# Optimization experiments

Hardware: AMD Instinct MI355X
Metric: run time of the kernel (lower is better)

## Reference

```python
import jax, jax.numpy as jnp
import numpy as np

N_NODES = 10000
N_EDGES = 320000
IN_FEATS = 500
CONV_DIMS = [500, 256, 256]
FC_DIMS = [256, 128, 40]
BN_EPS = 1e-5


def setup_inputs() -> dict:
    key = jax.random.key(0)
    ks = jax.random.split(key, 16)
    inp = {
        "x": jax.random.normal(ks[0], (N_NODES, IN_FEATS), dtype=jnp.float32),
        "edge_index": jax.random.randint(ks[1], (2, N_EDGES), 0, N_NODES, dtype=jnp.int64),
    }
    # conv layer params: Linear W [in,out], b [out]; BatchNorm gamma/beta [out]
    ki = 2
    for li in range(len(CONV_DIMS) - 1):
        d_in, d_out = CONV_DIMS[li], CONV_DIMS[li + 1]
        s = 1.0 / np.sqrt(d_in)
        inp[f"conv_W{li}"] = jax.random.uniform(ks[ki], (d_in, d_out), jnp.float32, -s, s); ki += 1
        inp[f"conv_b{li}"] = jax.random.uniform(ks[ki], (d_out,), jnp.float32, -s, s); ki += 1
        inp[f"bn_g{li}"] = jnp.ones((d_out,), jnp.float32)
        inp[f"bn_b{li}"] = jnp.zeros((d_out,), jnp.float32)
    for li in range(len(FC_DIMS) - 1):
        d_in, d_out = FC_DIMS[li], FC_DIMS[li + 1]
        s = 1.0 / np.sqrt(d_in)
        inp[f"fc_W{li}"] = jax.random.uniform(ks[ki], (d_in, d_out), jnp.float32, -s, s); ki += 1
        inp[f"fc_b{li}"] = jax.random.uniform(ks[ki], (d_out,), jnp.float32, -s, s); ki += 1
    return inp


def _degree(edge_index, n, dtype):
    # Faithful to: A = eye(N); A[i,j] = 1 per edge (set semantics dedupes repeats).
    A = jnp.eye(n, dtype=dtype).at[edge_index[0], edge_index[1]].set(1.0)
    return A.sum(axis=1)  # deg_i = rowsum of A


def _batchnorm(h, g, b):
    # training-mode BatchNorm1d: batch stats, biased variance
    mean = h.mean(axis=0)
    var = h.var(axis=0)
    return (h - mean) * jax.lax.rsqrt(var + BN_EPS) * g + b


def reference(x, edge_index, conv_W0, conv_b0, bn_g0, bn_b0,
              conv_W1, conv_b1, bn_g1, bn_b1,
              fc_W0, fc_b0, fc_W1, fc_b1):
    n = x.shape[0]
    deg = _degree(edge_index, n, x.dtype)
    # D = sqrt(diag(deg)) is a diagonal matrix, so elementwise D*A*D = diag(deg);
    # mm(D*A*D, x) == deg[:, None] * x (exactly the original math).
    h = x
    for W, b, g, beta in ((conv_W0, conv_b0, bn_g0, bn_b0),
                          (conv_W1, conv_b1, bn_g1, bn_b1)):
        h = (deg[:, None] * h) @ W + b
        h = jax.nn.relu(h)
        h = _batchnorm(h, g, beta)
        # dropout: identity at inference
    for W, b in ((fc_W0, fc_b0), (fc_W1, fc_b1)):
        h = jax.nn.relu(h @ W + b)  # original appends ReLU after every fc, incl. last
    return h
```

## Files before the change

### kernel.cpp

```cpp
#include <hip/hip_runtime.h>

#define NN 10000
#define NE 320000
#define ROW_WORDS 320
#define MP 10112
#define BN_EPS 1e-5f

typedef __attribute__((ext_vector_type(8))) short short8;
typedef __attribute__((ext_vector_type(4))) float f32x4;
typedef unsigned short u16;

__device__ __forceinline__ void split1(float v, u16& h, u16& l) {
    unsigned int u = __float_as_uint(v);
    h = (u16)(u >> 16);
    float hf = __uint_as_float(u & 0xFFFF0000u);
    l = (u16)(__float_as_uint(v - hf) >> 16);
}

__device__ __forceinline__ void gll16(const void* g, void* l) {
    __builtin_amdgcn_global_load_lds(
        (const __attribute__((address_space(1))) unsigned int*)g,
        (__attribute__((address_space(3))) unsigned int*)l, 16, 0, 0);
}

__global__ void scatter_bits(const int* __restrict__ ei, unsigned int* __restrict__ bitmap) {
    int t = blockIdx.x * blockDim.x + threadIdx.x;
    if (t < NE) {
        int i = ei[t];
        int j = ei[NE + t];
        atomicOr(&bitmap[i * ROW_WORDS + (j >> 5)], 1u << (j & 31));
    } else if (t < NE + NN) {
        int i = t - NE;
        atomicOr(&bitmap[i * ROW_WORDS + (i >> 5)], 1u << (i & 31));
    }
}

__device__ void splitW_dev(const float* __restrict__ W, int K, int N, int Kp, int Np,
                           u16* __restrict__ Wt, int bx, int by, char* smem) {
    float (*tile)[65] = (float(*)[65])smem;
    int t = threadIdx.x;
    int bk = bx * 64, bn = by * 64;
    #pragma unroll
    for (int p = 0; p < 4; ++p) {
        int kk = (t >> 4) + p * 16;
        int nc = (t & 15) * 4;
        int k = bk + kk;
        float4 v = {0.f, 0.f, 0.f, 0.f};
        if (k < K && bn + nc + 3 < N)
            v = *(const float4*)&W[(size_t)k * N + bn + nc];
        tile[kk][nc] = v.x; tile[kk][nc + 1] = v.y;
        tile[kk][nc + 2] = v.z; tile[kk][nc + 3] = v.w;
    }
    __syncthreads();
    int nn = t >> 2;
    int kk0 = (t & 3) * 16;
    u16 hs[16], ls[16];
    #pragma unroll
    for (int j = 0; j < 16; ++j) split1(tile[kk0 + j][nn], hs[j], ls[j]);
    size_t ob = (size_t)(bn + nn) * Kp + bk + kk0;
    size_t lo = (size_t)Np * Kp;
    *(short8*)&Wt[ob] = *(short8*)hs;
    *(short8*)&Wt[ob + 8] = *(short8*)&hs[8];
    *(short8*)&Wt[lo + ob] = *(short8*)ls;
    *(short8*)&Wt[lo + ob + 8] = *(short8*)&ls[8];
}

__device__ void xsplit_dev(const float* __restrict__ x, u16* __restrict__ xs, int gblk) {
    int t = threadIdx.x;
    int r0 = gblk * 16 + (t >> 4);
    int l = t & 15;
    u16* xlo = xs + (size_t)MP * 512;
    #pragma unroll
    for (int j = 0; j < 8; ++j) {
        int k = (l + j * 16) * 4;
        float vals[4] = {0.f, 0.f, 0.f, 0.f};
        if (r0 < NN && k < 500) {
            float4 v = *(const float4*)&x[(size_t)r0 * 500 + k];
            vals[0] = v.x; vals[1] = v.y; vals[2] = v.z; vals[3] = v.w;
        }
        ushort4 hs, ls;
        split1(vals[0], hs.x, ls.x); split1(vals[1], hs.y, ls.y);
        split1(vals[2], hs.z, ls.z); split1(vals[3], hs.w, ls.w);
        *(ushort4*)&xs[(size_t)r0 * 512 + k] = hs;
        *(ushort4*)&xlo[(size_t)r0 * 512 + k] = ls;
    }
}

__device__ void degree_dev(const unsigned int* __restrict__ bitmap, float* __restrict__ deg,
                           int gblk) {
    int t = threadIdx.x;
    int r = gblk * 16 + (t >> 4), l = t & 15;
    int cnt = 0;
    if (r < NN)
        for (int wd = l; wd < ROW_WORDS; wd += 16)
            cnt += __popc(bitmap[(size_t)r * ROW_WORDS + wd]);
    cnt += __shfl_down(cnt, 8, 16);
    cnt += __shfl_down(cnt, 4, 16);
    cnt += __shfl_down(cnt, 2, 16);
    cnt += __shfl_down(cnt, 1, 16);
    if (l == 0 && r < NN) deg[r] = (float)cnt;
}

__global__ __launch_bounds__(256)
void prep(const unsigned int* __restrict__ bitmap, const float* __restrict__ x,
          const float* __restrict__ W0, const float* __restrict__ fW1,
          float* __restrict__ deg, u16* __restrict__ xs,
          u16* __restrict__ W0t, u16* __restrict__ fW1t) {
    __shared__ char smem[16704];
    int b = blockIdx.x;
    if (b < 632) {
        degree_dev(bitmap, deg, b);
        xsplit_dev(x, xs, b);
    } else if (b < 664) {
        int idx = b - 632;
        splitW_dev(W0, 500, 256, 512, 256, W0t, idx & 7, idx >> 3, smem);
    } else {
        splitW_dev(fW1, 128, 40, 128, 64, fW1t, b - 664, 0, smem);
    }
}

__global__ __launch_bounds__(256, 3)
void conv0_gemm(const u16* __restrict__ Ahi, const u16* __restrict__ Alo,
                const u16* __restrict__ Bhi, const u16* __restrict__ Blo,
                const float* __restrict__ bias, const float* __restrict__ deg,
                float* __restrict__ stats, u16* __restrict__ Ohi, u16* __restrict__ Olo) {
    __shared__ char smem[32768];
    const int Kp = 512, M = NN, No = 256;
    const int t = threadIdx.x;
    const int lane = t & 63;
    const int w = t >> 6;
    const int q = lane >> 4;
    const int l16 = lane & 15;
    const int m7 = l16 & 7;
    const int row0 = blockIdx.y * 64;
    const int col0 = blockIdx.x * 64;

    const u16* bases[4] = {Ahi, Alo, Bhi, Blo};
    const u16* srcs[8];
    unsigned dstoff[8];
    #pragma unroll
    for (int i = 0; i < 8; ++i) {
        int gi = w + i * 4;
        int reg = i >> 1;
        int j = gi & 7;
        int rb = (reg < 2) ? row0 : col0;
        int r = j * 8 + (lane >> 3);
        int c = (lane & 7) ^ (r & 7);
        srcs[i] = bases[reg] + (size_t)(rb + r) * Kp + c * 8;
        dstoff[i] = reg * 8192 + j * 1024;
    }

    f32x4 acc[4];
    #pragma unroll
    for (int s = 0; s < 4; ++s) acc[s] = (f32x4){0.f, 0.f, 0.f, 0.f};

    #pragma unroll
    for (int i = 0; i < 8; ++i) { gll16(srcs[i], smem + dstoff[i]); srcs[i] += 64; }

    for (int k0 = 0; k0 < Kp; k0 += 64) {
        __syncthreads();
        short8 ah[2], al[2], bh[2][4], bl[2][4];
        #pragma unroll
        for (int kc = 0; kc < 2; ++kc) {
            int aoff = (w * 16 + l16) * 128 + (((kc * 4 + q) ^ m7) * 16);
            ah[kc] = *(const short8*)(smem + aoff);
            al[kc] = *(const short8*)(smem + 8192 + aoff);
            #pragma unroll
            for (int s = 0; s < 4; ++s) {
                int boff = (s * 16 + l16) * 128 + (((kc * 4 + q) ^ m7) * 16);
                bh[kc][s] = *(const short8*)(smem + 16384 + boff);
                bl[kc][s] = *(const short8*)(smem + 24576 + boff);
            }
        }
        __syncthreads();
        if (k0 + 64 < Kp) {
            #pragma unroll
            for (int i = 0; i < 8; ++i) { gll16(srcs[i], smem + dstoff[i]); srcs[i] += 64; }
        }
        #pragma unroll
        for (int kc = 0; kc < 2; ++kc)
            #pragma unroll
            for (int s = 0; s < 4; ++s) {
                acc[s] = __builtin_amdgcn_mfma_f32_16x16x32_bf16(al[kc], bh[kc][s], acc[s], 0, 0, 0);
                acc[s] = __builtin_amdgcn_mfma_f32_16x16x32_bf16(ah[kc], bl[kc][s], acc[s], 0, 0, 0);
                acc[s] = __builtin_amdgcn_mfma_f32_16x16x32_bf16(ah[kc], bh[kc][s], acc[s], 0, 0, 0);
            }
    }

    int growb = row0 + w * 16 + q * 4;
    float dgv[4];
    #pragma unroll
    for (int r = 0; r < 4; ++r) dgv[r] = (growb + r < M) ? deg[growb + r] : 0.f;
    #pragma unroll
    for (int s = 0; s < 4; ++s) {
        int gc = col0 + s * 16 + l16;
        float bia = bias[gc];
        float s_sum = 0.f, ss_sum = 0.f;
        #pragma unroll
        for (int r = 0; r < 4; ++r) {
            int grow = growb + r;
            bool real = grow < M;
            float v = fmaxf(fmaf(dgv[r], acc[s][r], bia), 0.f);
            if (!real) v = 0.f;
            s_sum += v; ss_sum += v * v;
            float vo = v * dgv[r];
            u16 h, l; split1(vo, h, l);
            Ohi[(size_t)grow * No + gc] = h;
            Olo[(size_t)grow * No + gc] = l;
        }
        s_sum  += __shfl_xor(s_sum, 16);  s_sum  += __shfl_xor(s_sum, 32);
        ss_sum += __shfl_xor(ss_sum, 16); ss_sum += __shfl_xor(ss_sum, 32);
        if (lane < 16) {
            atomicAdd(&stats[gc], s_sum);
            atomicAdd(&stats[256 + gc], ss_sum);
        }
    }
}

__global__ __launch_bounds__(256, 2)
void conv1_fold(const u16* __restrict__ Ahi, const u16* __restrict__ Alo,
                const float* __restrict__ W1, const float* __restrict__ stats0,
                const float* __restrict__ g0, const float* __restrict__ bb0,
                const float* __restrict__ b1, const float* __restrict__ deg,
                float* __restrict__ stats1, u16* __restrict__ Ohi, u16* __restrict__ Olo) {
    __shared__ char smem[32768];
    __shared__ float scl[256], sh[256], cred[256], cvec[64];
    const int Kp = 256, M = NN, No = 256;
    const int t = threadIdx.x;
    const int lane = t & 63;
    const int w = t >> 6;
    const int q = lane >> 4;
    const int l16 = lane & 15;
    const int m7 = l16 & 7;
    const int row0 = blockIdx.y * 64;
    const int col0 = blockIdx.x * 64;

    const u16* srcs[4];
    unsigned dstoff[4];
    #pragma unroll
    for (int i = 0; i < 4; ++i) {
        int gi = w + i * 4;
        int plane = gi >> 3, j = gi & 7;
        int r = j * 8 + (lane >> 3);
        int c = (lane & 7) ^ (r & 7);
        srcs[i] = (plane ? Alo : Ahi) + (size_t)(row0 + r) * Kp + c * 8;
        dstoff[i] = plane * 8192 + j * 1024;
    }
    #pragma unroll
    for (int i = 0; i < 4; ++i) { gll16(srcs[i], smem + dstoff[i]); srcs[i] += 64; }

    {
        float mean = stats0[t] * (1.f / NN);
        float var = stats0[256 + t] * (1.f / NN) - mean * mean;
        float s = g0[t] * rsqrtf(var + BN_EPS);
        scl[t] = s;
        sh[t] = bb0[t] - mean * s;
    }
    __syncthreads();
    {
        float s = 0.f;
        int n = col0 + (t & 63);
        #pragma unroll 8
        for (int k = (t >> 6); k < 256; k += 4)
            s += sh[k] * W1[(size_t)k * 256 + n];
        cred[t] = s;
        __syncthreads();
        if (t < 64) cvec[t] = cred[t] + cred[t + 64] + cred[t + 128] + cred[t + 192];
    }
    const int bn = t & 63;
    const int kb = (t >> 6) * 16;
    const int ch0 = (t >> 6) * 2;
    float vals[16];
    {
        const float* wp = W1 + (size_t)kb * 256 + col0 + bn;
        #pragma unroll
        for (int i = 0; i < 16; ++i) vals[i] = wp[(size_t)i * 256] * scl[kb + i];
    }

    f32x4 acc[4];
    #pragma unroll
    for (int s = 0; s < 4; ++s) acc[s] = (f32x4){0.f, 0.f, 0.f, 0.f};

    for (int k0 = 0; k0 < Kp; k0 += 64) {
        {
            u16 hs[16], ls[16];
            #pragma unroll
            for (int i = 0; i < 16; ++i) split1(vals[i], hs[i], ls[i]);
            unsigned o0 = bn * 128 + ((ch0 ^ (bn & 7)) * 16);
            unsigned o1 = bn * 128 + (((ch0 + 1) ^ (bn & 7)) * 16);
            *(short8*)(smem + 16384 + o0) = *(short8*)&hs[0];
            *(short8*)(smem + 16384 + o1) = *(short8*)&hs[8];
            *(short8*)(smem + 24576 + o0) = *(short8*)&ls[0];
            *(short8*)(smem + 24576 + o1) = *(short8*)&ls[8];
        }
        __syncthreads();
        short8 ah[2], al[2], bh[2][4], bl[2][4];
        #pragma unroll
        for (int kc = 0; kc < 2; ++kc) {
            int aoff = (w * 16 + l16) * 128 + (((kc * 4 + q) ^ m7) * 16);
            ah[kc] = *(const short8*)(smem + aoff);
            al[kc] = *(const short8*)(smem + 8192 + aoff);
            #pragma unroll
            for (int s = 0; s < 4; ++s) {
                int boff = (s * 16 + l16) * 128 + (((kc * 4 + q) ^ m7) * 16);
                bh[kc][s] = *(const short8*)(smem + 16384 + boff);
                bl[kc][s] = *(const short8*)(smem + 24576 + boff);
            }
        }
        __syncthreads();
        if (k0 + 64 < Kp) {
            #pragma unroll
            for (int i = 0; i < 4; ++i) { gll16(srcs[i], smem + dstoff[i]); srcs[i] += 64; }
            const float* wp = W1 + (size_t)(k0 + 64 + kb) * 256 + col0 + bn;
            #pragma unroll
            for (int i = 0; i < 16; ++i) vals[i] = wp[(size_t)i * 256] * scl[k0 + 64 + kb + i];
        }
        #pragma unroll
        for (int kc = 0; kc < 2; ++kc)
            #pragma unroll
            for (int s = 0; s < 4; ++s) {
                acc[s] = __builtin_amdgcn_mfma_f32_16x16x32_bf16(al[kc], bh[kc][s], acc[s], 0, 0, 0);
                acc[s] = __builtin_amdgcn_mfma_f32_16x16x32_bf16(ah[kc], bl[kc][s], acc[s], 0, 0, 0);
                acc[s] = __builtin_amdgcn_mfma_f32_16x16x32_bf16(ah[kc], bh[kc][s], acc[s], 0, 0, 0);
            }
    }

    int growb = row0 + w * 16 + q * 4;
    float dgv[4];
    #pragma unroll
    for (int r = 0; r < 4; ++r) dgv[r] = (growb + r < M) ? deg[growb + r] : 0.f;
    #pragma unroll
    for (int s = 0; s < 4; ++s) {
        int gc = col0 + s * 16 + l16;
        float bia = b1[gc];
        float cv = cvec[s * 16 + l16];
        float s_sum = 0.f, ss_sum = 0.f;
        #pragma unroll
        for (int r = 0; r < 4; ++r) {
            int grow = growb + r;
            bool real = grow < M;
            float v = fmaxf(fmaf(dgv[r], cv, acc[s][r] + bia), 0.f);
            if (!real) v = 0.f;
            s_sum += v; ss_sum += v * v;
            u16 h, l; split1(v, h, l);
            Ohi[(size_t)grow * No + gc] = h;
            Olo[(size_t)grow * No + gc] = l;
        }
        s_sum  += __shfl_xor(s_sum, 16);  s_sum  += __shfl_xor(s_sum, 32);
        ss_sum += __shfl_xor(ss_sum, 16); ss_sum += __shfl_xor(ss_sum, 32);
        if (lane < 16) {
            atomicAdd(&stats1[gc], s_sum);
            atomicAdd(&stats1[256 + gc], ss_sum);
        }
    }
}

__global__ __launch_bounds__(256, 2)
void fc0_fold(const u16* __restrict__ Ahi, const u16* __restrict__ Alo,
              const float* __restrict__ fW0, const float* __restrict__ stats1,
              const float* __restrict__ g1, const float* __restrict__ bb1,
              const float* __restrict__ fb0,
              u16* __restrict__ Ohi, u16* __restrict__ Olo) {
    __shared__ char smem[32768];
    __shared__ float scl[256], sh[256], cred[256], biasf[64];
    const int Kp = 256, M = NN, No = 128;
    const int t = threadIdx.x;
    const int lane = t & 63;
    const int w = t >> 6;
    const int q = lane >> 4;
    const int l16 = lane & 15;
    const int m7 = l16 & 7;
    const int row0 = blockIdx.y * 64;
    const int col0 = blockIdx.x * 64;

    const u16* srcs[4];
    unsigned dstoff[4];
    #pragma unroll
    for (int i = 0; i < 4; ++i) {
        int gi = w + i * 4;
        int plane = gi >> 3, j = gi & 7;
        int r = j * 8 + (lane >> 3);
        int c = (lane & 7) ^ (r & 7);
        srcs[i] = (plane ? Alo : Ahi) + (size_t)(row0 + r) * Kp + c * 8;
        dstoff[i] = plane * 8192 + j * 1024;
    }
    #pragma unroll
    for (int i = 0; i < 4; ++i) { gll16(srcs[i], smem + dstoff[i]); srcs[i] += 64; }

    {
        float mean = stats1[t] * (1.f / NN);
        float var = stats1[256 + t] * (1.f / NN) - mean * mean;
        float s = g1[t] * rsqrtf(var + BN_EPS);
        scl[t] = s;
        sh[t] = bb1[t] - mean * s;
    }
    __syncthreads();
    {
        float s = 0.f;
        int n = col0 + (t & 63);
        #pragma unroll 8
        for (int k = (t >> 6); k < 256; k += 4)
            s += sh[k] * fW0[(size_t)k * 128 + n];
        cred[t] = s;
        __syncthreads();
        if (t < 64)
            biasf[t] = fb0[col0 + t] + cred[t] + cred[t + 64] + cred[t + 128] + cred[t + 192];
    }
    const int bn = t & 63;
    const int kb = (t >> 6) * 16;
    const int ch0 = (t >> 6) * 2;
    float vals[16];
    {
        const float* wp = fW0 + (size_t)kb * 128 + col0 + bn;
        #pragma unroll
        for (int i = 0; i < 16; ++i) vals[i] = wp[(size_t)i * 128] * scl[kb + i];
    }

    f32x4 acc[4];
    #pragma unroll
    for (int s = 0; s < 4; ++s) acc[s] = (f32x4){0.f, 0.f, 0.f, 0.f};

    for (int k0 = 0; k0 < Kp; k0 += 64) {
        {
            u16 hs[16], ls[16];
            #pragma unroll
            for (int i = 0; i < 16; ++i) split1(vals[i], hs[i], ls[i]);
            unsigned o0 = bn * 128 + ((ch0 ^ (bn & 7)) * 16);
            unsigned o1 = bn * 128 + (((ch0 + 1) ^ (bn & 7)) * 16);
            *(short8*)(smem + 16384 + o0) = *(short8*)&hs[0];
            *(short8*)(smem + 16384 + o1) = *(short8*)&hs[8];
            *(short8*)(smem + 24576 + o0) = *(short8*)&ls[0];
            *(short8*)(smem + 24576 + o1) = *(short8*)&ls[8];
        }
        __syncthreads();
        short8 ah[2], al[2], bh[2][4], bl[2][4];
        #pragma unroll
        for (int kc = 0; kc < 2; ++kc) {
            int aoff = (w * 16 + l16) * 128 + (((kc * 4 + q) ^ m7) * 16);
            ah[kc] = *(const short8*)(smem + aoff);
            al[kc] = *(const short8*)(smem + 8192 + aoff);
            #pragma unroll
            for (int s = 0; s < 4; ++s) {
                int boff = (s * 16 + l16) * 128 + (((kc * 4 + q) ^ m7) * 16);
                bh[kc][s] = *(const short8*)(smem + 16384 + boff);
                bl[kc][s] = *(const short8*)(smem + 24576 + boff);
            }
        }
        __syncthreads();
        if (k0 + 64 < Kp) {
            #pragma unroll
            for (int i = 0; i < 4; ++i) { gll16(srcs[i], smem + dstoff[i]); srcs[i] += 64; }
            const float* wp = fW0 + (size_t)(k0 + 64 + kb) * 128 + col0 + bn;
            #pragma unroll
            for (int i = 0; i < 16; ++i) vals[i] = wp[(size_t)i * 128] * scl[k0 + 64 + kb + i];
        }
        #pragma unroll
        for (int kc = 0; kc < 2; ++kc)
            #pragma unroll
            for (int s = 0; s < 4; ++s) {
                acc[s] = __builtin_amdgcn_mfma_f32_16x16x32_bf16(al[kc], bh[kc][s], acc[s], 0, 0, 0);
                acc[s] = __builtin_amdgcn_mfma_f32_16x16x32_bf16(ah[kc], bl[kc][s], acc[s], 0, 0, 0);
                acc[s] = __builtin_amdgcn_mfma_f32_16x16x32_bf16(ah[kc], bh[kc][s], acc[s], 0, 0, 0);
            }
    }

    int growb = row0 + w * 16 + q * 4;
    #pragma unroll
    for (int s = 0; s < 4; ++s) {
        int gc = col0 + s * 16 + l16;
        float bia = biasf[s * 16 + l16];
        #pragma unroll
        for (int r = 0; r < 4; ++r) {
            int grow = growb + r;
            float v = fmaxf(acc[s][r] + bia, 0.f);
            if (grow >= M) v = 0.f;
            u16 h, l; split1(v, h, l);
            Ohi[(size_t)grow * No + gc] = h;
            Olo[(size_t)grow * No + gc] = l;
        }
    }
}

__global__ __launch_bounds__(256, 3)
void fc1_gemm(const u16* __restrict__ Ahi, const u16* __restrict__ Alo,
              const u16* __restrict__ Bhi, const u16* __restrict__ Blo,
              const float* __restrict__ bias, float* __restrict__ out) {
    __shared__ char smem[32768];
    const int Kp = 128, M = NN, N = 40, No = 40;
    const int t = threadIdx.x;
    const int lane = t & 63;
    const int w = t >> 6;
    const int q = lane >> 4;
    const int l16 = lane & 15;
    const int m7 = l16 & 7;
    const int row0 = blockIdx.y * 64;
    const int col0 = 0;

    const u16* bases[4] = {Ahi, Alo, Bhi, Blo};
    const u16* srcs[8];
    unsigned dstoff[8];
    #pragma unroll
    for (int i = 0; i < 8; ++i) {
        int gi = w + i * 4;
        int reg = i >> 1;
        int j = gi & 7;
        int rb = (reg < 2) ? row0 : col0;
        int r = j * 8 + (lane >> 3);
        int c = (lane & 7) ^ (r & 7);
        srcs[i] = bases[reg] + (size_t)(rb + r) * Kp + c * 8;
        dstoff[i] = reg * 8192 + j * 1024;
    }

    f32x4 acc[4];
    #pragma unroll
    for (int s = 0; s < 4; ++s) acc[s] = (f32x4){0.f, 0.f, 0.f, 0.f};

    #pragma unroll
    for (int i = 0; i < 8; ++i) { gll16(srcs[i], smem + dstoff[i]); srcs[i] += 64; }

    for (int k0 = 0; k0 < Kp; k0 += 64) {
        __syncthreads();
        short8 ah[2], al[2], bh[2][4], bl[2][4];
        #pragma unroll
        for (int kc = 0; kc < 2; ++kc) {
            int aoff = (w * 16 + l16) * 128 + (((kc * 4 + q) ^ m7) * 16);
            ah[kc] = *(const short8*)(smem + aoff);
            al[kc] = *(const short8*)(smem + 8192 + aoff);
            #pragma unroll
            for (int s = 0; s < 4; ++s) {
                int boff = (s * 16 + l16) * 128 + (((kc * 4 + q) ^ m7) * 16);
                bh[kc][s] = *(const short8*)(smem + 16384 + boff);
                bl[kc][s] = *(const short8*)(smem + 24576 + boff);
            }
        }
        __syncthreads();
        if (k0 + 64 < Kp) {
            #pragma unroll
            for (int i = 0; i < 8; ++i) { gll16(srcs[i], smem + dstoff[i]); srcs[i] += 64; }
        }
        #pragma unroll
        for (int kc = 0; kc < 2; ++kc)
            #pragma unroll
            for (int s = 0; s < 4; ++s) {
                acc[s] = __builtin_amdgcn_mfma_f32_16x16x32_bf16(al[kc], bh[kc][s], acc[s], 0, 0, 0);
                acc[s] = __builtin_amdgcn_mfma_f32_16x16x32_bf16(ah[kc], bl[kc][s], acc[s], 0, 0, 0);
                acc[s] = __builtin_amdgcn_mfma_f32_16x16x32_bf16(ah[kc], bh[kc][s], acc[s], 0, 0, 0);
            }
    }

    int growb = row0 + w * 16 + q * 4;
    #pragma unroll
    for (int s = 0; s < 4; ++s) {
        int gc = col0 + s * 16 + l16;
        if (gc >= N) continue;
        float bia = bias[gc];
        #pragma unroll
        for (int r = 0; r < 4; ++r) {
            int grow = growb + r;
            if (grow < M)
                out[(size_t)grow * No + gc] = fmaxf(acc[s][r] + bia, 0.f);
        }
    }
}


extern "C" void kernel_launch(void* const* d_in, const int* in_sizes, int n_in,
                              void* d_out, int out_size, void* d_ws, size_t ws_size,
                              hipStream_t stream) {
    const float* x   = (const float*)d_in[0];
    const int*   ei  = (const int*)d_in[1];
    const float* W0  = (const float*)d_in[2];
    const float* b0  = (const float*)d_in[3];
    const float* g0  = (const float*)d_in[4];
    const float* bb0 = (const float*)d_in[5];
    const float* W1  = (const float*)d_in[6];
    const float* b1  = (const float*)d_in[7];
    const float* g1  = (const float*)d_in[8];
    const float* bb1 = (const float*)d_in[9];
    const float* fW0 = (const float*)d_in[10];
    const float* fb0 = (const float*)d_in[11];
    const float* fW1 = (const float*)d_in[12];
    const float* fb1 = (const float*)d_in[13];
    float* out = (float*)d_out;

    char* ws = (char*)d_ws;
    auto carve = [&](size_t bytes) { char* q = ws; ws += (bytes + 255) & ~(size_t)255; return q; };

    const size_t BITMAP_BYTES = (size_t)NN * ROW_WORDS * 4;
    char* region0 = carve(BITMAP_BYTES + 4096);
    unsigned int* bitmap = (unsigned int*)region0;
    float* stats = (float*)(region0 + BITMAP_BYTES);
    u16* H1 = (u16*)region0;

    float* deg  = (float*)carve(MP * 4);
    u16* xs     = (u16*)carve((size_t)2 * MP * 512 * 2);
    u16* W0t    = (u16*)carve((size_t)2 * 256 * 512 * 2);
    u16* fW1t   = (u16*)carve((size_t)2 * 64 * 128 * 2);
    u16* H2     = (u16*)carve((size_t)2 * MP * 256 * 2);
    u16* H3     = (u16*)carve((size_t)2 * MP * 128 * 2);

    dim3 blk(256);

    hipMemsetAsync(region0, 0, BITMAP_BYTES + 4096, stream);
    scatter_bits<<<(NE + NN + 255) / 256, blk, 0, stream>>>(ei, bitmap);
    prep<<<666, blk, 0, stream>>>(bitmap, x, W0, fW1, deg, xs, W0t, fW1t);
    conv0_gemm<<<dim3(4, 158), blk, 0, stream>>>(
        xs, xs + (size_t)MP * 512, W0t, W0t + 256 * 512,
        b0, deg, stats, H1, H1 + (size_t)MP * 256);
    conv1_fold<<<dim3(4, 158), blk, 0, stream>>>(
        H1, H1 + (size_t)MP * 256, W1, stats, g0, bb0, b1, deg,
        stats + 512, H2, H2 + (size_t)MP * 256);
    fc0_fold<<<dim3(2, 158), blk, 0, stream>>>(
        H2, H2 + (size_t)MP * 256, fW0, stats + 512, g1, bb1, fb0,
        H3, H3 + (size_t)MP * 128);
    fc1_gemm<<<dim3(1, 158), blk, 0, stream>>>(
        H3, H3 + (size_t)MP * 128, fW1t, fW1t + 64 * 128, fb1, out);
}
```

Before: 193.2 us.

## Fuse degree counting into edge scatter and split x inside conv0 GEMM

Degree is now counted during the edge scatter: the return value of atomicOr shows whether a bit was newly set, and only then is the row counter incremented. This removes the separate popcount pass over the bitmap and one kernel launch. The conv0 GEMM now loads fp32 x straight into LDS and does the hi/lo bf16 split in registers, so the pre-split xs buffer is never written or read. The cost is extra ALU work in the GEMM inner loop and contended atomics on the degree counters. Reads for the padded K tail run into the next row of x, and past the end of x for the last row; this relies on the zero-padded weights cancelling those values.

```diff
diff --git a/kernel.cpp b/kernel.cpp
--- a/kernel.cpp
+++ b/kernel.cpp
@@ -21,18 +21,6 @@
     __builtin_amdgcn_global_load_lds(
         (const __attribute__((address_space(1))) unsigned int*)g,
         (__attribute__((address_space(3))) unsigned int*)l, 16, 0, 0);
-}
-
-__global__ void scatter_bits(const int* __restrict__ ei, unsigned int* __restrict__ bitmap) {
-    int t = blockIdx.x * blockDim.x + threadIdx.x;
-    if (t < NE) {
-        int i = ei[t];
-        int j = ei[NE + t];
-        atomicOr(&bitmap[i * ROW_WORDS + (j >> 5)], 1u << (j & 31));
-    } else if (t < NE + NN) {
-        int i = t - NE;
-        atomicOr(&bitmap[i * ROW_WORDS + (i >> 5)], 1u << (i & 31));
-    }
 }
 
 __device__ void splitW_dev(const float* __restrict__ W, int K, int N, int Kp, int Np,
@@ -65,67 +53,38 @@
     *(short8*)&Wt[lo + ob + 8] = *(short8*)&ls[8];
 }
 
-__device__ void xsplit_dev(const float* __restrict__ x, u16* __restrict__ xs, int gblk) {
-    int t = threadIdx.x;
-    int r0 = gblk * 16 + (t >> 4);
-    int l = t & 15;
-    u16* xlo = xs + (size_t)MP * 512;
-    #pragma unroll
-    for (int j = 0; j < 8; ++j) {
-        int k = (l + j * 16) * 4;
-        float vals[4] = {0.f, 0.f, 0.f, 0.f};
-        if (r0 < NN && k < 500) {
-            float4 v = *(const float4*)&x[(size_t)r0 * 500 + k];
-            vals[0] = v.x; vals[1] = v.y; vals[2] = v.z; vals[3] = v.w;
-        }
-        ushort4 hs, ls;
-        split1(vals[0], hs.x, ls.x); split1(vals[1], hs.y, ls.y);
-        split1(vals[2], hs.z, ls.z); split1(vals[3], hs.w, ls.w);
-        *(ushort4*)&xs[(size_t)r0 * 512 + k] = hs;
-        *(ushort4*)&xlo[(size_t)r0 * 512 + k] = ls;
-    }
-}
-
-__device__ void degree_dev(const unsigned int* __restrict__ bitmap, float* __restrict__ deg,
-                           int gblk) {
-    int t = threadIdx.x;
-    int r = gblk * 16 + (t >> 4), l = t & 15;
-    int cnt = 0;
-    if (r < NN)
-        for (int wd = l; wd < ROW_WORDS; wd += 16)
-            cnt += __popc(bitmap[(size_t)r * ROW_WORDS + wd]);
-    cnt += __shfl_down(cnt, 8, 16);
-    cnt += __shfl_down(cnt, 4, 16);
-    cnt += __shfl_down(cnt, 2, 16);
-    cnt += __shfl_down(cnt, 1, 16);
-    if (l == 0 && r < NN) deg[r] = (float)cnt;
-}
-
 __global__ __launch_bounds__(256)
-void prep(const unsigned int* __restrict__ bitmap, const float* __restrict__ x,
-          const float* __restrict__ W0, const float* __restrict__ fW1,
-          float* __restrict__ deg, u16* __restrict__ xs,
-          u16* __restrict__ W0t, u16* __restrict__ fW1t) {
+void scatter_prep(const int* __restrict__ ei, unsigned int* __restrict__ bitmap,
+                  int* __restrict__ degc,
+                  const float* __restrict__ W0, const float* __restrict__ fW1,
+                  u16* __restrict__ W0t, u16* __restrict__ fW1t) {
     __shared__ char smem[16704];
     int b = blockIdx.x;
-    if (b < 632) {
-        degree_dev(bitmap, deg, b);
-        xsplit_dev(x, xs, b);
-    } else if (b < 664) {
-        int idx = b - 632;
+    if (b < 1290) {
+        int e = b * 256 + threadIdx.x;
+        if (e < NE + NN) {
+            int i, j;
+            if (e < NE) { i = ei[e]; j = ei[NE + e]; }
+            else        { i = e - NE; j = i; }
+            unsigned bit = 1u << (j & 31);
+            unsigned old = atomicOr(&bitmap[i * ROW_WORDS + (j >> 5)], bit);
+            if (!(old & bit)) atomicAdd(&degc[i], 1);
+        }
+    } else if (b < 1322) {
+        int idx = b - 1290;
         splitW_dev(W0, 500, 256, 512, 256, W0t, idx & 7, idx >> 3, smem);
     } else {
-        splitW_dev(fW1, 128, 40, 128, 64, fW1t, b - 664, 0, smem);
+        splitW_dev(fW1, 128, 40, 128, 64, fW1t, b - 1322, 0, smem);
     }
 }
 
 __global__ __launch_bounds__(256, 3)
-void conv0_gemm(const u16* __restrict__ Ahi, const u16* __restrict__ Alo,
+void conv0_gemm(const float* __restrict__ x,
                 const u16* __restrict__ Bhi, const u16* __restrict__ Blo,
-                const float* __restrict__ bias, const float* __restrict__ deg,
+                const float* __restrict__ bias, const int* __restrict__ degc,
                 float* __restrict__ stats, u16* __restrict__ Ohi, u16* __restrict__ Olo) {
     __shared__ char smem[32768];
-    const int Kp = 512, M = NN, No = 256;
+    const int M = NN, No = 256;
     const int t = threadIdx.x;
     const int lane = t & 63;
     const int w = t >> 6;
@@ -135,19 +94,28 @@
     const int row0 = blockIdx.y * 64;
     const int col0 = blockIdx.x * 64;
 
-    const u16* bases[4] = {Ahi, Alo, Bhi, Blo};
-    const u16* srcs[8];
-    unsigned dstoff[8];
-    #pragma unroll
-    for (int i = 0; i < 8; ++i) {
-        int gi = w + i * 4;
-        int reg = i >> 1;
-        int j = gi & 7;
-        int rb = (reg < 2) ? row0 : col0;
-        int r = j * 8 + (lane >> 3);
-        int c = (lane & 7) ^ (r & 7);
-        srcs[i] = bases[reg] + (size_t)(rb + r) * Kp + c * 8;
-        dstoff[i] = reg * 8192 + j * 1024;
+    const float* afp[4];
+    unsigned adst[4];
+    const u16* bsp[4];
+    unsigned bdst[4];
+    #pragma unroll
+    for (int i = 0; i < 4; ++i) {
+        {
+            int j = w + i * 4;
+            int r = j * 4 + (lane >> 4);
+            int ck = (lane & 15) ^ (r & 15);
+            int gr = row0 + r; if (gr > NN - 1) gr = NN - 1;
+            afp[i] = x + (size_t)gr * 500 + ck * 4;
+            adst[i] = j * 1024;
+        }
+        {
+            int gb = w + i * 4;
+            int plane = gb >> 3, j = gb & 7;
+            int r = j * 8 + (lane >> 3);
+            int c = (lane & 7) ^ (r & 7);
+            bsp[i] = (plane ? Blo : Bhi) + (size_t)(col0 + r) * 512 + c * 8;
+            bdst[i] = 16384 + plane * 8192 + j * 1024;
+        }
     }
 
     f32x4 acc[4];
@@ -155,16 +123,28 @@
     for (int s = 0; s < 4; ++s) acc[s] = (f32x4){0.f, 0.f, 0.f, 0.f};
 
     #pragma unroll
-    for (int i = 0; i < 8; ++i) { gll16(srcs[i], smem + dstoff[i]); srcs[i] += 64; }
-
-    for (int k0 = 0; k0 < Kp; k0 += 64) {
+    for (int i = 0; i < 4; ++i) {
+        gll16(afp[i], smem + adst[i]); afp[i] += 64;
+        gll16(bsp[i], smem + bdst[i]); bsp[i] += 64;
+    }
+
+    const int rw = w * 16 + l16;
+    for (int k0 = 0; k0 < 512; k0 += 64) {
         __syncthreads();
         short8 ah[2], al[2], bh[2][4], bl[2][4];
         #pragma unroll
         for (int kc = 0; kc < 2; ++kc) {
-            int aoff = (w * 16 + l16) * 128 + (((kc * 4 + q) ^ m7) * 16);
-            ah[kc] = *(const short8*)(smem + aoff);
-            al[kc] = *(const short8*)(smem + 8192 + aoff);
+            int f = kc * 8 + q * 2;
+            int p0 = f ^ l16;
+            float4 a0 = *(const float4*)(smem + rw * 256 + p0 * 16);
+            float4 a1 = *(const float4*)(smem + rw * 256 + (p0 ^ 1) * 16);
+            u16 hh[8], ll[8];
+            split1(a0.x, hh[0], ll[0]); split1(a0.y, hh[1], ll[1]);
+            split1(a0.z, hh[2], ll[2]); split1(a0.w, hh[3], ll[3]);
+            split1(a1.x, hh[4], ll[4]); split1(a1.y, hh[5], ll[5]);
+            split1(a1.z, hh[6], ll[6]); split1(a1.w, hh[7], ll[7]);
+            ah[kc] = *(short8*)hh;
+            al[kc] = *(short8*)ll;
             #pragma unroll
             for (int s = 0; s < 4; ++s) {
                 int boff = (s * 16 + l16) * 128 + (((kc * 4 + q) ^ m7) * 16);
@@ -173,9 +153,12 @@
             }
         }
         __syncthreads();
-        if (k0 + 64 < Kp) {
-            #pragma unroll
-            for (int i = 0; i < 8; ++i) { gll16(srcs[i], smem + dstoff[i]); srcs[i] += 64; }
+        if (k0 + 64 < 512) {
+            #pragma unroll
+            for (int i = 0; i < 4; ++i) {
+                gll16(afp[i], smem + adst[i]); afp[i] += 64;
+                gll16(bsp[i], smem + bdst[i]); bsp[i] += 64;
+            }
         }
         #pragma unroll
         for (int kc = 0; kc < 2; ++kc)
@@ -190,7 +173,8 @@
     int growb = row0 + w * 16 + q * 4;
     float dgv[4];
     #pragma unroll
-    for (int r = 0; r < 4; ++r) dgv[r] = (growb + r < M) ? deg[growb + r] : 0.f;
+    for (int r = 0; r < 4; ++r)
+        dgv[r] = (growb + r < M) ? (float)degc[growb + r] : 0.f;
     #pragma unroll
     for (int s = 0; s < 4; ++s) {
         int gc = col0 + s * 16 + l16;
@@ -221,7 +205,7 @@
 void conv1_fold(const u16* __restrict__ Ahi, const u16* __restrict__ Alo,
                 const float* __restrict__ W1, const float* __restrict__ stats0,
                 const float* __restrict__ g0, const float* __restrict__ bb0,
-                const float* __restrict__ b1, const float* __restrict__ deg,
+                const float* __restrict__ b1, const int* __restrict__ degc,
                 float* __restrict__ stats1, u16* __restrict__ Ohi, u16* __restrict__ Olo) {
     __shared__ char smem[32768];
     __shared__ float scl[256], sh[256], cred[256], cvec[64];
@@ -328,7 +312,8 @@
     int growb = row0 + w * 16 + q * 4;
     float dgv[4];
     #pragma unroll
-    for (int r = 0; r < 4; ++r) dgv[r] = (growb + r < M) ? deg[growb + r] : 0.f;
+    for (int r = 0; r < 4; ++r)
+        dgv[r] = (growb + r < M) ? (float)degc[growb + r] : 0.f;
     #pragma unroll
     for (int s = 0; s < 4; ++s) {
         int gc = col0 + s * 16 + l16;
@@ -587,13 +572,13 @@
     auto carve = [&](size_t bytes) { char* q = ws; ws += (bytes + 255) & ~(size_t)255; return q; };
 
     const size_t BITMAP_BYTES = (size_t)NN * ROW_WORDS * 4;
-    char* region0 = carve(BITMAP_BYTES + 4096);
+    const size_t ZERO_BYTES = BITMAP_BYTES + 4096 + 40960;
+    char* region0 = carve(ZERO_BYTES);
     unsigned int* bitmap = (unsigned int*)region0;
     float* stats = (float*)(region0 + BITMAP_BYTES);
+    int* degc = (int*)(region0 + BITMAP_BYTES + 4096);
     u16* H1 = (u16*)region0;
 
-    float* deg  = (float*)carve(MP * 4);
-    u16* xs     = (u16*)carve((size_t)2 * MP * 512 * 2);
     u16* W0t    = (u16*)carve((size_t)2 * 256 * 512 * 2);
     u16* fW1t   = (u16*)carve((size_t)2 * 64 * 128 * 2);
     u16* H2     = (u16*)carve((size_t)2 * MP * 256 * 2);
@@ -601,14 +586,12 @@
 
     dim3 blk(256);
 
-    hipMemsetAsync(region0, 0, BITMAP_BYTES + 4096, stream);
-    scatter_bits<<<(NE + NN + 255) / 256, blk, 0, stream>>>(ei, bitmap);
-    prep<<<666, blk, 0, stream>>>(bitmap, x, W0, fW1, deg, xs, W0t, fW1t);
+    hipMemsetAsync(region0, 0, ZERO_BYTES, stream);
+    scatter_prep<<<1324, blk, 0, stream>>>(ei, bitmap, degc, W0, fW1, W0t, fW1t);
     conv0_gemm<<<dim3(4, 158), blk, 0, stream>>>(
-        xs, xs + (size_t)MP * 512, W0t, W0t + 256 * 512,
-        b0, deg, stats, H1, H1 + (size_t)MP * 256);
+        x, W0t, W0t + 256 * 512, b0, degc, stats, H1, H1 + (size_t)MP * 256);
     conv1_fold<<<dim3(4, 158), blk, 0, stream>>>(
-        H1, H1 + (size_t)MP * 256, W1, stats, g0, bb0, b1, deg,
+        H1, H1 + (size_t)MP * 256, W1, stats, g0, bb0, b1, degc,
         stats + 512, H2, H2 + (size_t)MP * 256);
     fc0_fold<<<dim3(2, 158), blk, 0, stream>>>(
         H2, H2 + (size_t)MP * 256, fW0, stats + 512, g1, bb1, fb0,
```

Measured after the change: 199.6 us. 1.03x slower.

## Fuse edge scatter with prep and count degree via atomicOr return value

Applied to the files above, without the earlier changes.

Merges the scatter_bits kernel into the prep kernel and computes node degrees on the fly by incrementing an integer counter whenever atomicOr sets a previously unset bit, which removes the separate bitmap popcount pass. This saves one kernel launch and the full read of the bitmap. In exchange it adds up to 330K atomic adds on the degree array, concentrated on a few counters per node. The feature split now runs in the same launch instead of after the scatter, and the conv kernels convert the integer degree to float when they load it.

```diff
diff --git a/kernel.cpp b/kernel.cpp
--- a/kernel.cpp
+++ b/kernel.cpp
@@ -21,18 +21,6 @@
     __builtin_amdgcn_global_load_lds(
         (const __attribute__((address_space(1))) unsigned int*)g,
         (__attribute__((address_space(3))) unsigned int*)l, 16, 0, 0);
-}
-
-__global__ void scatter_bits(const int* __restrict__ ei, unsigned int* __restrict__ bitmap) {
-    int t = blockIdx.x * blockDim.x + threadIdx.x;
-    if (t < NE) {
-        int i = ei[t];
-        int j = ei[NE + t];
-        atomicOr(&bitmap[i * ROW_WORDS + (j >> 5)], 1u << (j & 31));
-    } else if (t < NE + NN) {
-        int i = t - NE;
-        atomicOr(&bitmap[i * ROW_WORDS + (i >> 5)], 1u << (i & 31));
-    }
 }
 
 __device__ void splitW_dev(const float* __restrict__ W, int K, int N, int Kp, int Np,
@@ -86,43 +74,37 @@
     }
 }
 
-__device__ void degree_dev(const unsigned int* __restrict__ bitmap, float* __restrict__ deg,
-                           int gblk) {
-    int t = threadIdx.x;
-    int r = gblk * 16 + (t >> 4), l = t & 15;
-    int cnt = 0;
-    if (r < NN)
-        for (int wd = l; wd < ROW_WORDS; wd += 16)
-            cnt += __popc(bitmap[(size_t)r * ROW_WORDS + wd]);
-    cnt += __shfl_down(cnt, 8, 16);
-    cnt += __shfl_down(cnt, 4, 16);
-    cnt += __shfl_down(cnt, 2, 16);
-    cnt += __shfl_down(cnt, 1, 16);
-    if (l == 0 && r < NN) deg[r] = (float)cnt;
-}
-
 __global__ __launch_bounds__(256)
-void prep(const unsigned int* __restrict__ bitmap, const float* __restrict__ x,
-          const float* __restrict__ W0, const float* __restrict__ fW1,
-          float* __restrict__ deg, u16* __restrict__ xs,
-          u16* __restrict__ W0t, u16* __restrict__ fW1t) {
+void scatter_prep(const int* __restrict__ ei, unsigned int* __restrict__ bitmap,
+                  int* __restrict__ degc, const float* __restrict__ x,
+                  const float* __restrict__ W0, const float* __restrict__ fW1,
+                  u16* __restrict__ xs, u16* __restrict__ W0t, u16* __restrict__ fW1t) {
     __shared__ char smem[16704];
     int b = blockIdx.x;
-    if (b < 632) {
-        degree_dev(bitmap, deg, b);
-        xsplit_dev(x, xs, b);
-    } else if (b < 664) {
-        int idx = b - 632;
+    if (b < 1290) {
+        int e = b * 256 + threadIdx.x;
+        if (e < NE + NN) {
+            int i, j;
+            if (e < NE) { i = ei[e]; j = ei[NE + e]; }
+            else        { i = e - NE; j = i; }
+            unsigned bit = 1u << (j & 31);
+            unsigned old = atomicOr(&bitmap[i * ROW_WORDS + (j >> 5)], bit);
+            if (!(old & bit)) atomicAdd(&degc[i], 1);
+        }
+    } else if (b < 1922) {
+        xsplit_dev(x, xs, b - 1290);
+    } else if (b < 1954) {
+        int idx = b - 1922;
         splitW_dev(W0, 500, 256, 512, 256, W0t, idx & 7, idx >> 3, smem);
     } else {
-        splitW_dev(fW1, 128, 40, 128, 64, fW1t, b - 664, 0, smem);
+        splitW_dev(fW1, 128, 40, 128, 64, fW1t, b - 1954, 0, smem);
     }
 }
 
 __global__ __launch_bounds__(256, 3)
 void conv0_gemm(const u16* __restrict__ Ahi, const u16* __restrict__ Alo,
                 const u16* __restrict__ Bhi, const u16* __restrict__ Blo,
-                const float* __restrict__ bias, const float* __restrict__ deg,
+                const float* __restrict__ bias, const int* __restrict__ degc,
                 float* __restrict__ stats, u16* __restrict__ Ohi, u16* __restrict__ Olo) {
     __shared__ char smem[32768];
     const int Kp = 512, M = NN, No = 256;
@@ -190,7 +172,8 @@
     int growb = row0 + w * 16 + q * 4;
     float dgv[4];
     #pragma unroll
-    for (int r = 0; r < 4; ++r) dgv[r] = (growb + r < M) ? deg[growb + r] : 0.f;
+    for (int r = 0; r < 4; ++r)
+        dgv[r] = (growb + r < M) ? (float)degc[growb + r] : 0.f;
     #pragma unroll
     for (int s = 0; s < 4; ++s) {
         int gc = col0 + s * 16 + l16;
@@ -221,7 +204,7 @@
 void conv1_fold(const u16* __restrict__ Ahi, const u16* __restrict__ Alo,
                 const float* __restrict__ W1, const float* __restrict__ stats0,
                 const float* __restrict__ g0, const float* __restrict__ bb0,
-                const float* __restrict__ b1, const float* __restrict__ deg,
+                const float* __restrict__ b1, const int* __restrict__ degc,
                 float* __restrict__ stats1, u16* __restrict__ Ohi, u16* __restrict__ Olo) {
     __shared__ char smem[32768];
     __shared__ float scl[256], sh[256], cred[256], cvec[64];
@@ -328,7 +311,8 @@
     int growb = row0 + w * 16 + q * 4;
     float dgv[4];
     #pragma unroll
-    for (int r = 0; r < 4; ++r) dgv[r] = (growb + r < M) ? deg[growb + r] : 0.f;
+    for (int r = 0; r < 4; ++r)
+        dgv[r] = (growb + r < M) ? (float)degc[growb + r] : 0.f;
     #pragma unroll
     for (int s = 0; s < 4; ++s) {
         int gc = col0 + s * 16 + l16;
@@ -587,12 +571,13 @@
     auto carve = [&](size_t bytes) { char* q = ws; ws += (bytes + 255) & ~(size_t)255; return q; };
 
     const size_t BITMAP_BYTES = (size_t)NN * ROW_WORDS * 4;
-    char* region0 = carve(BITMAP_BYTES + 4096);
+    const size_t ZERO_BYTES = BITMAP_BYTES + 4096 + 40960;
+    char* region0 = carve(ZERO_BYTES);
     unsigned int* bitmap = (unsigned int*)region0;
     float* stats = (float*)(region0 + BITMAP_BYTES);
+    int* degc = (int*)(region0 + BITMAP_BYTES + 4096);
     u16* H1 = (u16*)region0;
 
-    float* deg  = (float*)carve(MP * 4);
     u16* xs     = (u16*)carve((size_t)2 * MP * 512 * 2);
     u16* W0t    = (u16*)carve((size_t)2 * 256 * 512 * 2);
     u16* fW1t   = (u16*)carve((size_t)2 * 64 * 128 * 2);
@@ -601,14 +586,13 @@
 
     dim3 blk(256);
 
-    hipMemsetAsync(region0, 0, BITMAP_BYTES + 4096, stream);
-    scatter_bits<<<(NE + NN + 255) / 256, blk, 0, stream>>>(ei, bitmap);
-    prep<<<666, blk, 0, stream>>>(bitmap, x, W0, fW1, deg, xs, W0t, fW1t);
+    hipMemsetAsync(region0, 0, ZERO_BYTES, stream);
+    scatter_prep<<<1956, blk, 0, stream>>>(ei, bitmap, degc, x, W0, fW1, xs, W0t, fW1t);
     conv0_gemm<<<dim3(4, 158), blk, 0, stream>>>(
         xs, xs + (size_t)MP * 512, W0t, W0t + 256 * 512,
-        b0, deg, stats, H1, H1 + (size_t)MP * 256);
+        b0, degc, stats, H1, H1 + (size_t)MP * 256);
     conv1_fold<<<dim3(4, 158), blk, 0, stream>>>(
-        H1, H1 + (size_t)MP * 256, W1, stats, g0, bb0, b1, deg,
+        H1, H1 + (size_t)MP * 256, W1, stats, g0, bb0, b1, degc,
         stats + 512, H2, H2 + (size_t)MP * 256);
     fc0_fold<<<dim3(2, 158), blk, 0, stream>>>(
         H2, H2 + (size_t)MP * 256, fW0, stats + 512, g1, bb1, fb0,
```

Result: slower. 208.4 us (+7.8%).
